# Optimization experiments

Hardware: AMD Instinct MI355X
Metric: run time of the kernel (lower is better)

The kernel has to match this reference:

```python
import jax, jax.numpy as jnp
from jax import lax
import numpy as np

B, C, H, W = 8, 192, 128, 128
HEADS, WS, SS = 6, 8, 4
HID = 768  # 4 * C
HEAD_DIM = C // HEADS
SCALE = HEAD_DIM ** -0.5
EPS = 1e-5


def _rel_pos_index(ws):
    coords = np.stack(np.meshgrid(np.arange(ws), np.arange(ws), indexing='ij'))  # (2, ws, ws)
    flat = coords.reshape(2, ws * ws)
    rel = flat[:, :, None] - flat[:, None, :]          # (2, N, N)
    rel = rel.transpose(1, 2, 0)                       # (N, N, 2)
    rel[:, :, 0] += ws - 1
    rel[:, :, 1] += ws - 1
    rel[:, :, 0] *= 2 * ws - 1
    return rel.sum(-1).astype(np.int32)                # (N, N)


def _attn_mask(hp, wp, ws, ss):
    # Swin shift mask: 0 where tokens share a region, -100 otherwise. (nW, N, N)
    img = np.zeros((hp, wp), dtype=np.float32)
    slices = (slice(0, -ws), slice(-ws, -ss), slice(-ss, None))
    cnt = 0
    for hs in slices:
        for ws_ in slices:
            img[hs, ws_] = float(cnt)
            cnt += 1
    mw = img.reshape(hp // ws, ws, wp // ws, ws).transpose(0, 2, 1, 3).reshape(-1, ws * ws)
    am = mw[:, None, :] - mw[:, :, None]
    return np.where(am != 0, -100.0, 0.0).astype(np.float32)


def _layernorm(x, g, b):
    mu = jnp.mean(x, axis=-1, keepdims=True)
    var = jnp.mean(jnp.square(x - mu), axis=-1, keepdims=True)
    return (x - mu) * lax.rsqrt(var + EPS) * g + b


def setup_inputs() -> dict:
    key = jax.random.key(0)
    ks = jax.random.split(key, 16)
    s = 0.02
    return {
        'x': jax.random.normal(ks[0], (B, C, H, W), jnp.float32),
        'pos_conv_w': jax.random.normal(ks[1], (C, 1, 3, 3), jnp.float32) * s,
        'norm1_g': jnp.ones((C,), jnp.float32),
        'norm1_b': jnp.zeros((C,), jnp.float32),
        'qkv_w': jax.random.normal(ks[2], (C, 3 * C), jnp.float32) * s,
        'qkv_b': jnp.zeros((3 * C,), jnp.float32),
        'proj_w': jax.random.normal(ks[3], (C, C), jnp.float32) * s,
        'proj_b': jnp.zeros((C,), jnp.float32),
        'rel_bias_table': jax.random.normal(ks[4], ((2 * WS - 1) ** 2, HEADS), jnp.float32) * s,
        'norm2_g': jnp.ones((C,), jnp.float32),
        'norm2_b': jnp.zeros((C,), jnp.float32),
        'mlp_w1': jax.random.normal(ks[5], (C, HID), jnp.float32) * s,
        'mlp_b1': jnp.zeros((HID,), jnp.float32),
        'mlp_w2': jax.random.normal(ks[6], (HID, C), jnp.float32) * s,
        'mlp_b2': jnp.zeros((C,), jnp.float32),
    }


def reference(x, pos_conv_w, norm1_g, norm1_b, qkv_w, qkv_b, proj_w, proj_b,
              rel_bias_table, norm2_g, norm2_b, mlp_w1, mlp_b1, mlp_w2, mlp_b2):
    b, c, h, w = x.shape
    ws, ss, nh, hd = WS, SS, HEADS, HEAD_DIM
    N = ws * ws

    # depthwise 3x3 positional conv (residual)
    x = x + lax.conv_general_dilated(
        x, pos_conv_w, (1, 1), 'SAME', feature_group_count=c,
        dimension_numbers=('NCHW', 'OIHW', 'NCHW'))

    if ss > 0:
        x = jnp.roll(x, (-ss, -ss), axis=(2, 3))

    pad_h = (ws - h % ws) % ws
    pad_w = (ws - w % ws) % ws
    if pad_h or pad_w:
        x = jnp.pad(x, ((0, 0), (0, 0), (0, pad_h), (0, pad_w)))
    hp, wp = h + pad_h, w + pad_w

    # window partition -> (num_windows, N, c)
    windows = x.reshape(b, c, hp // ws, ws, wp // ws, ws)
    windows = windows.transpose(0, 2, 4, 3, 5, 1).reshape(-1, N, c)
    nw = windows.shape[0]

    a = _layernorm(windows, norm1_g, norm1_b)
    qkv = (a @ qkv_w + qkv_b).reshape(nw, N, 3, nh, hd).transpose(2, 0, 3, 1, 4)
    q, k, v = qkv[0], qkv[1], qkv[2]                      # (nw, nh, N, hd)

    attn = jnp.einsum('whnd,whmd->whnm', q * SCALE, k)    # (nw, nh, N, N)

    rel_idx = jnp.asarray(_rel_pos_index(ws))             # (N, N) int
    bias = rel_bias_table[rel_idx.reshape(-1)].reshape(N, N, nh).transpose(2, 0, 1)
    attn = attn + bias[None]

    if ss > 0:
        mask = jnp.asarray(_attn_mask(hp, wp, ws, ss))    # (nW_per_img, N, N)
        nwpb = (hp // ws) * (wp // ws)
        attn = attn.reshape(b, nwpb, nh, N, N) + mask[None, :, None]
        attn = attn.reshape(nw, nh, N, N)

    attn = jax.nn.softmax(attn, axis=-1)
    out = jnp.einsum('whnm,whmd->whnd', attn, v).transpose(0, 2, 1, 3).reshape(nw, N, c)

    windows = windows + out @ proj_w + proj_b
    hmid = jax.nn.gelu(_layernorm(windows, norm2_g, norm2_b) @ mlp_w1 + mlp_b1, approximate=False)
    windows = windows + hmid @ mlp_w2 + mlp_b2

    # unpartition -> (b, c, hp, wp), crop, roll back
    y = windows.reshape(b, hp // ws, wp // ws, ws, ws, c)
    y = y.transpose(0, 5, 1, 3, 2, 4).reshape(b, c, hp, wp)[:, :, :h, :w]
    if ss > 0:
        y = jnp.roll(y, (ss, ss), axis=(2, 3))
    return y
```

## Files before the change

### kernel.cpp

```cpp
#include <hip/hip_runtime.h>
#include <hip/hip_bf16.h>
#include <cstdint>
#include <cstddef>

typedef short short8 __attribute__((ext_vector_type(8)));
typedef float float4_ __attribute__((ext_vector_type(4)));
typedef unsigned int uint4_ __attribute__((ext_vector_type(4)));
typedef unsigned int uint2_ __attribute__((ext_vector_type(2)));

#define DEVI static __device__ __forceinline__

DEVI unsigned short f2bf(float f) {
  union { float f; unsigned u; } v; v.f = f;
  return (unsigned short)((v.u + 0x7FFFu + ((v.u >> 16) & 1u)) >> 16);
}
DEVI unsigned pack2bf(float a, float b) {
  return (unsigned)f2bf(a) | ((unsigned)f2bf(b) << 16);
}
DEVI unsigned short f2bfc(float f) {
  __hip_bfloat16 h = __float2bfloat16(f);
  union { __hip_bfloat16 h1; unsigned short u; } cv; cv.h1 = h; return cv.u;
}
DEVI unsigned pack2bfc(float a, float b) {
  float2 f2; f2.x = a; f2.y = b;
  __hip_bfloat162 h = __float22bfloat162_rn(f2);
  union { __hip_bfloat162 h2; unsigned u; } cv; cv.h2 = h; return cv.u;
}
DEVI float bf2f(unsigned short h) {
  union { unsigned u; float f; } v; v.u = ((unsigned)h) << 16;
  return v.f;
}
DEVI float gelu_f(float x) {
  float u = x * (0.7978845608f + 0.0356774081f * x * x);
  float e = exp2f(-2.8853900818f * u);
  return x * __builtin_amdgcn_rcpf(1.0f + e);
}

#define SCALE_Q 0.17677669529663687f

__global__ __launch_bounds__(256) void k_prep(
    const float* __restrict__ qkv_w, const float* __restrict__ qkv_b,
    const float* __restrict__ proj_w, const float* __restrict__ mlp_w1,
    const float* __restrict__ mlp_w2, const float* __restrict__ relt,
    unsigned short* __restrict__ qkvWT, unsigned short* __restrict__ projWT,
    unsigned short* __restrict__ w1T, unsigned short* __restrict__ w2T,
    float* __restrict__ qkv_b_s, float* __restrict__ bias_attn) {
  int i = blockIdx.x * 256 + threadIdx.x;
  if (i < 110592) { int n = i / 192, k = i - n * 192;
    float v = qkv_w[k * 576 + n]; if (n < 192) v *= SCALE_Q;
    qkvWT[i] = f2bf(v); return; }
  i -= 110592;
  if (i < 576) { qkv_b_s[i] = qkv_b[i] * (i < 192 ? SCALE_Q : 1.0f); return; }
  i -= 576;
  if (i < 36864) { int n = i / 192, k = i - n * 192;
    projWT[i] = f2bf(proj_w[k * 192 + n]); return; }
  i -= 36864;
  if (i < 147456) { int n = i / 192, k = i - n * 192;
    w1T[i] = f2bf(mlp_w1[k * 768 + n]); return; }
  i -= 147456;
  if (i < 147456) { int n = i / 768, k = i - n * 768;
    w2T[i] = f2bf(mlp_w2[k * 192 + n]); return; }
  i -= 147456;
  if (i < 24576) {
    int h = i >> 12, nm = i & 4095, n = nm >> 6, m = nm & 63;
    int dr = (n >> 3) - (m >> 3) + 7, dc = (n & 7) - (m & 7) + 7;
    bias_attn[i] = relt[(dr * 15 + dc) * 6 + h];
  }
}

__global__ __launch_bounds__(256) void k_conv(
    const float* __restrict__ x, const float* __restrict__ convw,
    unsigned short* __restrict__ temp) {
  __shared__ float s_in[66 * 128];
  int bx = blockIdx.x;
  int c = bx >> 1, seg = bx & 1, b = blockIdx.y;
  int h0 = seg * 64;
  int t = threadIdx.x;
  const float* xp = x + ((size_t)(b * 192 + c)) * 16384;
  #pragma unroll
  for (int i = 0; i < 9; ++i) {
    int q = t + i * 256;
    if (q < 2112) {
      int srow = q >> 5, chunk = q & 31;
      float4_ v = *(const float4_*)(xp + ((h0 + 3 + srow) & 127) * 128 + chunk * 4);
      *(float4_*)(s_in + srow * 128 + chunk * 4) = v;
    }
  }
  float cw9[9];
  #pragma unroll
  for (int i = 0; i < 9; ++i) cw9[i] = convw[c * 9 + i];
  __syncthreads();
  int r2 = t >> 7;
  int wp = t & 127;
  int w_true = (wp + 4) & 127;
  float mw0 = (w_true != 0) ? 1.f : 0.f;
  float mw2 = (w_true != 127) ? 1.f : 0.f;
  int wl0 = (w_true + 127) & 127, wl2 = (w_true + 1) & 127;
  unsigned short* tp = temp + ((size_t)(b * 192 + c)) * 16384;
  #pragma unroll 4
  for (int it = 0; it < 32; ++it) {
    int r = it * 2 + r2;
    int h_true = (h0 + 4 + r) & 127;
    float mh0 = (h_true != 0) ? 1.f : 0.f;
    float mh2 = (h_true != 127) ? 1.f : 0.f;
    const float* row0 = s_in + r * 128;
    const float* row1 = row0 + 128;
    const float* row2 = row1 + 128;
    float acc = row1[w_true];
    acc = fmaf(cw9[0], mh0 * mw0 * row0[wl0], acc);
    acc = fmaf(cw9[1], mh0 * row0[w_true], acc);
    acc = fmaf(cw9[2], mh0 * mw2 * row0[wl2], acc);
    acc = fmaf(cw9[3], mw0 * row1[wl0], acc);
    acc = fmaf(cw9[4], row1[w_true], acc);
    acc = fmaf(cw9[5], mw2 * row1[wl2], acc);
    acc = fmaf(cw9[6], mh2 * mw0 * row2[wl0], acc);
    acc = fmaf(cw9[7], mh2 * row2[w_true], acc);
    acc = fmaf(cw9[8], mh2 * mw2 * row2[wl2], acc);
    tp[(size_t)(h0 + r) * 128 + wp] = f2bf(acc);
  }
}

__global__ __launch_bounds__(256) void k_lnw(
    const unsigned short* __restrict__ temp, const float* __restrict__ g1,
    const float* __restrict__ b1, unsigned short* __restrict__ xw,
    unsigned short* __restrict__ a) {
  __shared__ unsigned short sT[192 * 128];
  __shared__ float s_g[192], s_b[192];
  int t = threadIdx.x;
  for (int i = t; i < 192; i += 256) { s_g[i] = g1[i]; s_b[i] = b1[i]; }
  int wj0 = blockIdx.x * 2, wi = blockIdx.y, b = blockIdx.z;
  const unsigned short* tb = temp + (size_t)b * (192 * 16384) + (wi * 8) * 128 + wj0 * 8;
  #pragma unroll
  for (int i = 0; i < 12; ++i) {
    int id = t + i * 256;
    int c = id >> 4, rem = id & 15, r = rem >> 1, piece = rem & 1;
    short8 v = *(const short8*)(tb + (size_t)c * 16384 + r * 128 + piece * 8);
    *(short8*)(sT + c * 128 + piece * 64 + r * 8) = v;
  }
  __syncthreads();
  int tok = t >> 1, half = t & 1, c0 = half * 96;
  size_t gtok = ((size_t)(b * 256 + wi * 16 + wj0 + (tok >> 6))) * 64 + (tok & 63);
  unsigned short* xwp = xw + gtok * 192 + c0;
  float sum = 0.f, sq = 0.f;
  #pragma unroll
  for (int j8 = 0; j8 < 12; ++j8) {
    unsigned short raw[8];
    unsigned pk[4];
    #pragma unroll
    for (int e = 0; e < 8; ++e) {
      unsigned short rv = sT[(c0 + j8 * 8 + e) * 128 + tok];
      raw[e] = rv;
      float x = bf2f(rv);
      sum += x; sq = fmaf(x, x, sq);
    }
    #pragma unroll
    for (int k = 0; k < 4; ++k) pk[k] = (unsigned)raw[2 * k] | ((unsigned)raw[2 * k + 1] << 16);
    uint4_ pv = { pk[0], pk[1], pk[2], pk[3] };
    *(uint4_*)(xwp + j8 * 8) = pv;
  }
  sum += __shfl_xor(sum, 1);
  sq  += __shfl_xor(sq, 1);
  float mu = sum * (1.f / 192.f);
  float var = sq * (1.f / 192.f) - mu * mu;
  float rs = rsqrtf(var + 1e-5f);
  unsigned short* ap = a + gtok * 192 + c0;
  #pragma unroll
  for (int j8 = 0; j8 < 12; ++j8) {
    unsigned pk[4];
    #pragma unroll
    for (int k = 0; k < 4; ++k) {
      int c = c0 + j8 * 8 + k * 2;
      float v0 = (bf2f(sT[c * 128 + tok]) - mu) * rs * s_g[c] + s_b[c];
      float v1 = (bf2f(sT[(c + 1) * 128 + tok]) - mu) * rs * s_g[c + 1] + s_b[c + 1];
      pk[k] = pack2bf(v0, v1);
    }
    uint4_ pv = { pk[0], pk[1], pk[2], pk[3] };
    *(uint4_*)(ap + j8 * 8) = pv;
  }
}

__global__ __launch_bounds__(384, 1) void k_qkvattn(
    const unsigned short* __restrict__ a, const unsigned short* __restrict__ wT,
    const float* __restrict__ qbias, const float* __restrict__ biasAll,
    unsigned short* __restrict__ outO) {
  __shared__ __align__(16) unsigned short sQK[6][4096];
  __shared__ __align__(16) unsigned short sVT[6][2048];
  int t = threadIdx.x, lane = t & 63, head = t / 64;
  int win = blockIdx.x;
  int wi = (win >> 4) & 15, wj = win & 15;
  int lrow = lane & 15, lkgrp = lane >> 4, lk = lkgrp * 8;
  const unsigned short* aWin = a + (size_t)win * (64 * 192);
  char* qk = (char*)sQK[head];
  char* vt = (char*)sVT[head];

  auto gemmQKV = [&](int sel) {
    const unsigned short* wb = wT + (size_t)(sel * 192 + head * 32) * 192;
    const float* bb = qbias + sel * 192 + head * 32;
    short8 bw[2][6];
    #pragma unroll
    for (int nb = 0; nb < 2; ++nb)
      #pragma unroll
      for (int ks = 0; ks < 6; ++ks)
        bw[nb][ks] = *(const short8*)(wb + (size_t)(nb * 16 + lrow) * 192 + ks * 32 + lk);
    float4_ acc[2][4];
    #pragma unroll
    for (int nb = 0; nb < 2; ++nb)
      #pragma unroll
      for (int mi = 0; mi < 4; ++mi) acc[nb][mi] = (float4_){0.f, 0.f, 0.f, 0.f};
    short8 af0[4], af1[4];
    #pragma unroll
    for (int mi = 0; mi < 4; ++mi)
      af0[mi] = *(const short8*)(aWin + (size_t)(mi * 16 + lrow) * 192 + lk);
    #pragma unroll
    for (int mi = 0; mi < 4; ++mi)
      af1[mi] = *(const short8*)(aWin + (size_t)(mi * 16 + lrow) * 192 + 32 + lk);
    #pragma unroll
    for (int ks = 0; ks < 6; ++ks) {
      #pragma unroll
      for (int mi = 0; mi < 4; ++mi) {
        short8 a_ = (ks & 1) ? af1[mi] : af0[mi];
        #pragma unroll
        for (int nb = 0; nb < 2; ++nb)
          acc[nb][mi] = __builtin_amdgcn_mfma_f32_16x16x32_bf16(bw[nb][ks], a_, acc[nb][mi], 0, 0, 0);
      }
      if (ks < 4) {
        #pragma unroll
        for (int mi = 0; mi < 4; ++mi) {
          short8 nv = *(const short8*)(aWin + (size_t)(mi * 16 + lrow) * 192 + (ks + 2) * 32 + lk);
          if (ks & 1) af1[mi] = nv; else af0[mi] = nv;
        }
      }
    }
    #pragma unroll
    for (int nb = 0; nb < 2; ++nb) {
      float4_ b4 = *(const float4_*)(bb + nb * 16 + lkgrp * 4);
      if (sel == 2) {
        #pragma unroll
        for (int mi = 0; mi < 4; ++mi) {
          int tok = mi * 16 + lrow;
          #pragma unroll
          for (int e = 0; e < 4; ++e) {
            int d = nb * 16 + lkgrp * 4 + e;
            *(unsigned short*)(vt + ((d * 128 + tok * 2) ^ ((d & 7) << 4))) =
                f2bfc(acc[nb][mi][e] + b4[e]);
          }
        }
      } else {
        int dsub2 = (nb * 16 + lkgrp * 4) * 2;
        #pragma unroll
        for (int mi = 0; mi < 4; ++mi) {
          int tok = mi * 16 + lrow;
          uint2_ pv = { pack2bfc(acc[nb][mi][0] + b4[0], acc[nb][mi][1] + b4[1]),
                        pack2bfc(acc[nb][mi][2] + b4[2], acc[nb][mi][3] + b4[3]) };
          *(uint2_*)(qk + sel * 4096 + ((tok * 64 + dsub2) ^ ((tok & 7) << 4))) = pv;
        }
      }
    }
  };
  gemmQKV(0);
  gemmQKV(1);
  gemmQKV(2);

  short8 kf[4];
  #pragma unroll
  for (int ni = 0; ni < 4; ++ni) {
    int tokk = ni * 16 + lrow;
    kf[ni] = *(const short8*)(qk + 4096 + ((tokk * 64 + lk * 2) ^ ((tokk & 7) << 4)));
  }
  float4_ s[4][4];
  __builtin_amdgcn_s_setprio(1);
  #pragma unroll
  for (int mi = 0; mi < 4; ++mi) {
    int tokq = mi * 16 + lrow;
    short8 qf = *(const short8*)(qk + ((tokq * 64 + lk * 2) ^ ((tokq & 7) << 4)));
    #pragma unroll
    for (int ni = 0; ni < 4; ++ni) {
      s[mi][ni] = (float4_){0.f, 0.f, 0.f, 0.f};
      s[mi][ni] = __builtin_amdgcn_mfma_f32_16x16x32_bf16(qf, kf[ni], s[mi][ni], 0, 0, 0);
    }
  }
  __builtin_amdgcn_s_setprio(0);
  const float* bh = biasAll + head * 4096;
  bool wi15 = (wi == 15), wj15 = (wj == 15);
  bool edge = wi15 || wj15;
  #pragma unroll
  for (int mi = 0; mi < 4; ++mi) {
    #pragma unroll
    for (int e = 0; e < 4; ++e) {
      int row = mi * 16 + lkgrp * 4 + e;
      int rcls = (wi15 ? ((row >> 3) >= 4 ? 2 : 1) : 0) * 3 +
                 (wj15 ? ((row & 7) >= 4 ? 2 : 1) : 0);
      float v[4];
      #pragma unroll
      for (int ni = 0; ni < 4; ++ni) {
        int col = ni * 16 + lrow;
        float xv = s[mi][ni][e] + bh[row * 64 + col];
        if (edge) {
          int ccls = (wi15 ? ((col >> 3) >= 4 ? 2 : 1) : 0) * 3 +
                     (wj15 ? ((col & 7) >= 4 ? 2 : 1) : 0);
          if (ccls != rcls) xv -= 100.f;
        }
        v[ni] = xv;
      }
      float mx = fmaxf(fmaxf(v[0], v[1]), fmaxf(v[2], v[3]));
      mx = fmaxf(mx, __shfl_xor(mx, 1));
      mx = fmaxf(mx, __shfl_xor(mx, 2));
      mx = fmaxf(mx, __shfl_xor(mx, 4));
      mx = fmaxf(mx, __shfl_xor(mx, 8));
      float sm = 0.f;
      #pragma unroll
      for (int ni = 0; ni < 4; ++ni) { v[ni] = __expf(v[ni] - mx); sm += v[ni]; }
      sm += __shfl_xor(sm, 1);
      sm += __shfl_xor(sm, 2);
      sm += __shfl_xor(sm, 4);
      sm += __shfl_xor(sm, 8);
      float inv = 1.f / sm;
      #pragma unroll
      for (int ni = 0; ni < 4; ++ni) {
        int col = ni * 16 + lrow;
        *(unsigned short*)(qk + ((row * 128 + col * 2) ^ ((row & 7) << 4))) = f2bfc(v[ni] * inv);
      }
    }
  }
  float4_ o[2][4];
  #pragma unroll
  for (int db = 0; db < 2; ++db)
    #pragma unroll
    for (int qb2 = 0; qb2 < 4; ++qb2) o[db][qb2] = (float4_){0.f, 0.f, 0.f, 0.f};
  __builtin_amdgcn_s_setprio(1);
  #pragma unroll
  for (int kk = 0; kk < 2; ++kk) {
    int ktok = kk * 32 + lk;
    short8 vf[2], pf[4];
    #pragma unroll
    for (int db = 0; db < 2; ++db) {
      int d = db * 16 + lrow;
      vf[db] = *(const short8*)(vt + ((d * 128 + ktok * 2) ^ ((d & 7) << 4)));
    }
    #pragma unroll
    for (int qb2 = 0; qb2 < 4; ++qb2) {
      int rq = qb2 * 16 + lrow;
      pf[qb2] = *(const short8*)(qk + ((rq * 128 + ktok * 2) ^ ((rq & 7) << 4)));
    }
    #pragma unroll
    for (int db = 0; db < 2; ++db)
      #pragma unroll
      for (int qb2 = 0; qb2 < 4; ++qb2)
        o[db][qb2] = __builtin_amdgcn_mfma_f32_16x16x32_bf16(vf[db], pf[qb2], o[db][qb2], 0, 0, 0);
  }
  __builtin_amdgcn_s_setprio(0);
  unsigned short* ob = outO + (size_t)win * (64 * 192);
  #pragma unroll
  for (int qb2 = 0; qb2 < 4; ++qb2)
    #pragma unroll
    for (int db = 0; db < 2; ++db) {
      unsigned lo = pack2bfc(o[db][qb2][0], o[db][qb2][1]);
      unsigned hi = pack2bfc(o[db][qb2][2], o[db][qb2][3]);
      uint2_ pv = { lo, hi };
      *(uint2_*)(ob + (size_t)(qb2 * 16 + lrow) * 192 + head * 32 + db * 16 + lkgrp * 4) = pv;
    }
}

__global__ __launch_bounds__(256, 2) void k_mlp(
    const unsigned short* __restrict__ O, const unsigned short* __restrict__ xw,
    const unsigned short* __restrict__ projWT, const float* __restrict__ proj_b,
    const float* __restrict__ n2g, const float* __restrict__ n2b,
    const unsigned short* __restrict__ w1T, const float* __restrict__ mlpb1,
    const unsigned short* __restrict__ w2T, const float* __restrict__ mlpb2,
    float* __restrict__ y) {
  __shared__ __align__(16) unsigned short sH[64 * 192];
  __shared__ __align__(16) unsigned short sB2[64 * 192];
  __shared__ float sRed[64 * 8];
  __shared__ unsigned sTok[64];
  int t = threadIdx.x, lane = t & 63, wn = t >> 6;
  int lrow = lane & 15, lkgrp = lane >> 4, lk = lkgrp * 8;
  int blk = blockIdx.x;
  int b = blk >> 8, rem = blk & 255, ta = rem >> 3, tb_ = rem & 7;
  if (t < 64) {
    int rr = t >> 4, ss = t & 15;
    int h = ta * 4 + rr, w = tb_ * 16 + ss;
    int hp = (h + 124) & 127, wp = (w + 124) & 127;
    unsigned gtok = ((unsigned)(b * 256 + (hp >> 3) * 16 + (wp >> 3))) * 64 +
                    (hp & 7) * 8 + (wp & 7);
    sTok[t] = gtok * 192u;
  }
  __syncthreads();
  unsigned aoff[4];
  #pragma unroll
  for (int mi = 0; mi < 4; ++mi) aoff[mi] = sTok[mi * 16 + lrow];
  float4_ tacc[4][3];
  #pragma unroll
  for (int mi = 0; mi < 4; ++mi)
    #pragma unroll
    for (int ni = 0; ni < 3; ++ni) tacc[mi][ni] = (float4_){0.f, 0.f, 0.f, 0.f};
  {
    short8 bP0[3][3], bP1[3][3], af0[4], af1[4];
    #pragma unroll
    for (int ni = 0; ni < 3; ++ni)
      #pragma unroll
      for (int k3 = 0; k3 < 3; ++k3)
        bP0[ni][k3] = *(const short8*)(projWT + (size_t)(wn * 48 + ni * 16 + lrow) * 192 + k3 * 32 + lk);
    #pragma unroll
    for (int mi = 0; mi < 4; ++mi)
      af0[mi] = *(const short8*)(O + aoff[mi] + lk);
    #pragma unroll
    for (int ni = 0; ni < 3; ++ni)
      #pragma unroll
      for (int k3 = 0; k3 < 3; ++k3)
        bP1[ni][k3] = *(const short8*)(projWT + (size_t)(wn * 48 + ni * 16 + lrow) * 192 + (3 + k3) * 32 + lk);
    #pragma unroll
    for (int mi = 0; mi < 4; ++mi)
      af1[mi] = *(const short8*)(O + aoff[mi] + 32 + lk);
    #pragma unroll
    for (int ks = 0; ks < 6; ++ks) {
      #pragma unroll
      for (int mi = 0; mi < 4; ++mi) {
        short8 a_ = (ks & 1) ? af1[mi] : af0[mi];
        #pragma unroll
        for (int ni = 0; ni < 3; ++ni) {
          short8 b_ = (ks < 3) ? bP0[ni][ks] : bP1[ni][ks - 3];
          tacc[mi][ni] = __builtin_amdgcn_mfma_f32_16x16x32_bf16(a_, b_, tacc[mi][ni], 0, 0, 0);
        }
      }
      if (ks < 4) {
        #pragma unroll
        for (int mi = 0; mi < 4; ++mi) {
          short8 nv = *(const short8*)(O + aoff[mi] + (ks + 2) * 32 + lk);
          if (ks & 1) af1[mi] = nv; else af0[mi] = nv;
        }
      }
    }
  }
  {
    unsigned roff[4][4];
    #pragma unroll
    for (int mi = 0; mi < 4; ++mi)
      #pragma unroll
      for (int e = 0; e < 4; ++e)
        roff[mi][e] = sTok[mi * 16 + lkgrp * 4 + e];
    unsigned short rxv[3][4][4];
    #pragma unroll
    for (int ni = 0; ni < 3; ++ni) {
      int col = wn * 48 + ni * 16 + lrow;
      #pragma unroll
      for (int mi = 0; mi < 4; ++mi)
        #pragma unroll
        for (int e = 0; e < 4; ++e)
          rxv[ni][mi][e] = xw[roff[mi][e] + col];
    }
    #pragma unroll
    for (int ni = 0; ni < 3; ++ni) {
      float pbv = proj_b[wn * 48 + ni * 16 + lrow];
      #pragma unroll
      for (int mi = 0; mi < 4; ++mi)
        #pragma unroll
        for (int e = 0; e < 4; ++e)
          tacc[mi][ni][e] += pbv + bf2f(rxv[ni][mi][e]);
    }
  }
  #pragma unroll
  for (int mi = 0; mi < 4; ++mi)
    #pragma unroll
    for (int e = 0; e < 4; ++e) {
      float s1 = tacc[mi][0][e] + tacc[mi][1][e] + tacc[mi][2][e];
      float s2 = tacc[mi][0][e] * tacc[mi][0][e] + tacc[mi][1][e] * tacc[mi][1][e] +
                 tacc[mi][2][e] * tacc[mi][2][e];
      s1 += __shfl_xor(s1, 1); s1 += __shfl_xor(s1, 2); s1 += __shfl_xor(s1, 4); s1 += __shfl_xor(s1, 8);
      s2 += __shfl_xor(s2, 1); s2 += __shfl_xor(s2, 2); s2 += __shfl_xor(s2, 4); s2 += __shfl_xor(s2, 8);
      if (lrow == 0) {
        int row = mi * 16 + lkgrp * 4 + e;
        sRed[row * 8 + wn * 2 + 0] = s1;
        sRed[row * 8 + wn * 2 + 1] = s2;
      }
    }
  __syncthreads();
  #pragma unroll
  for (int mi = 0; mi < 4; ++mi)
    #pragma unroll
    for (int e = 0; e < 4; ++e) {
      int row = mi * 16 + lkgrp * 4 + e;
      float s1 = sRed[row * 8] + sRed[row * 8 + 2] + sRed[row * 8 + 4] + sRed[row * 8 + 6];
      float s2 = sRed[row * 8 + 1] + sRed[row * 8 + 3] + sRed[row * 8 + 5] + sRed[row * 8 + 7];
      float mu = s1 * (1.f / 192.f);
      float var = s2 * (1.f / 192.f) - mu * mu;
      float rs = rsqrtf(var + 1e-5f);
      #pragma unroll
      for (int ni = 0; ni < 3; ++ni) {
        int col = wn * 48 + ni * 16 + lrow;
        float hv = (tacc[mi][ni][e] - mu) * rs * n2g[col] + n2b[col];
        *(unsigned short*)((char*)sH + ((row * 384 + col * 2) ^ ((row & 7) << 4))) = f2bfc(hv);
      }
    }
  __syncthreads();
  short8 bwA[6], bwB[6];
  #pragma unroll
  for (int ks = 0; ks < 6; ++ks)
    bwA[ks] = *(const short8*)(w1T + (size_t)(wn * 48 + lrow) * 192 + ks * 32 + lk);
  #pragma unroll 1
  for (int ch = 0; ch < 4; ++ch) {
    #pragma unroll 1
    for (int ni = 0; ni < 3; ++ni) {
      int nni = (ni < 2) ? ni + 1 : 0;
      int nch = (ni < 2) ? ch : ch + 1;
      if (nch < 4) {
        int gn = nch * 192 + wn * 48 + nni * 16 + lrow;
        #pragma unroll
        for (int ks = 0; ks < 6; ++ks)
          bwB[ks] = *(const short8*)(w1T + (size_t)gn * 192 + ks * 32 + lk);
      }
      float4_ h1[4];
      #pragma unroll
      for (int mi = 0; mi < 4; ++mi) h1[mi] = (float4_){0.f, 0.f, 0.f, 0.f};
      __builtin_amdgcn_s_setprio(1);
      #pragma unroll
      for (int ks = 0; ks < 6; ++ks) {
        int kb = ks * 32 + lk;
        #pragma unroll
        for (int mi = 0; mi < 4; ++mi) {
          int row = mi * 16 + lrow;
          short8 afv = *(const short8*)((const char*)sH + ((row * 384 + kb * 2) ^ ((row & 7) << 4)));
          h1[mi] = __builtin_amdgcn_mfma_f32_16x16x32_bf16(bwA[ks], afv, h1[mi], 0, 0, 0);
        }
      }
      __builtin_amdgcn_s_setprio(0);
      float4_ b4 = *(const float4_*)(mlpb1 + ch * 192 + wn * 48 + ni * 16 + lkgrp * 4);
      int nsub2 = (wn * 48 + ni * 16 + lkgrp * 4) * 2;
      #pragma unroll
      for (int mi = 0; mi < 4; ++mi) {
        int tok_ = mi * 16 + lrow;
        float g0 = gelu_f(h1[mi][0] + b4[0]);
        float g1 = gelu_f(h1[mi][1] + b4[1]);
        float g2 = gelu_f(h1[mi][2] + b4[2]);
        float g3 = gelu_f(h1[mi][3] + b4[3]);
        uint2_ pv = { pack2bfc(g0, g1), pack2bfc(g2, g3) };
        *(uint2_*)((char*)sB2 + ((tok_ * 384 + nsub2) ^ ((tok_ & 7) << 4))) = pv;
      }
      #pragma unroll
      for (int ks = 0; ks < 6; ++ks) bwA[ks] = bwB[ks];
    }
    short8 cw0[3][3], cw1[3][3];
    #pragma unroll
    for (int ni = 0; ni < 3; ++ni)
      #pragma unroll
      for (int k3 = 0; k3 < 3; ++k3)
        cw0[ni][k3] = *(const short8*)(w2T + (size_t)(wn * 48 + ni * 16 + lrow) * 768 + ch * 192 + k3 * 32 + lk);
    __syncthreads();
    #pragma unroll
    for (int ni = 0; ni < 3; ++ni)
      #pragma unroll
      for (int k3 = 0; k3 < 3; ++k3)
        cw1[ni][k3] = *(const short8*)(w2T + (size_t)(wn * 48 + ni * 16 + lrow) * 768 + ch * 192 + (3 + k3) * 32 + lk);
    __builtin_amdgcn_s_setprio(1);
    #pragma unroll
    for (int ks = 0; ks < 6; ++ks) {
      int kb = ks * 32 + lk;
      short8 af[4];
      #pragma unroll
      for (int mi = 0; mi < 4; ++mi) {
        int row = mi * 16 + lrow;
        af[mi] = *(const short8*)((const char*)sB2 + ((row * 384 + kb * 2) ^ ((row & 7) << 4)));
      }
      #pragma unroll
      for (int mi = 0; mi < 4; ++mi)
        #pragma unroll
        for (int ni = 0; ni < 3; ++ni) {
          short8 b_ = (ks < 3) ? cw0[ni][ks] : cw1[ni][ks - 3];
          tacc[mi][ni] = __builtin_amdgcn_mfma_f32_16x16x32_bf16(af[mi], b_, tacc[mi][ni], 0, 0, 0);
        }
    }
    __builtin_amdgcn_s_setprio(0);
    __syncthreads();
  }
  int wcol = tb_ * 16 + lkgrp * 4;
  #pragma unroll
  for (int ni = 0; ni < 3; ++ni) {
    int col = wn * 48 + ni * 16 + lrow;
    float b2v = mlpb2[col];
    #pragma unroll
    for (int mi = 0; mi < 4; ++mi) {
      int h = ta * 4 + mi;
      float4_ vv;
      #pragma unroll
      for (int e = 0; e < 4; ++e) vv[e] = tacc[mi][ni][e] + b2v;
      *(float4_*)(y + ((size_t)(b * 192 + col) * 128 + h) * 128 + wcol) = vv;
    }
  }
}

extern "C" void kernel_launch(void* const* d_in, const int* in_sizes, int n_in,
                              void* d_out, int out_size, void* d_ws, size_t ws_size,
                              hipStream_t stream) {
  (void)in_sizes; (void)n_in; (void)out_size;
  const float* x    = (const float*)d_in[0];
  const float* pcw  = (const float*)d_in[1];
  const float* n1g  = (const float*)d_in[2];
  const float* n1b  = (const float*)d_in[3];
  const float* qkvw = (const float*)d_in[4];
  const float* qkvb = (const float*)d_in[5];
  const float* pw   = (const float*)d_in[6];
  const float* pb   = (const float*)d_in[7];
  const float* relt = (const float*)d_in[8];
  const float* n2g  = (const float*)d_in[9];
  const float* n2b  = (const float*)d_in[10];
  const float* w1   = (const float*)d_in[11];
  const float* mb1  = (const float*)d_in[12];
  const float* w2   = (const float*)d_in[13];
  const float* mb2  = (const float*)d_in[14];
  float* y = (float*)d_out;
  char* ws = (char*)d_ws;
  size_t off = 0;
  auto carve = [&](size_t bytes) { void* p = ws + off; off += (bytes + 255) & ~(size_t)255; return p; };
  unsigned short* qkvWT  = (unsigned short*)carve(576 * 192 * 2);
  unsigned short* projWT = (unsigned short*)carve(192 * 192 * 2);
  unsigned short* w1T    = (unsigned short*)carve(768 * 192 * 2);
  unsigned short* w2T    = (unsigned short*)carve(192 * 768 * 2);
  float* qkv_b_s   = (float*)carve(576 * 4);
  float* bias_attn = (float*)carve(6 * 64 * 64 * 4);
  unsigned short* aBuf   = (unsigned short*)carve((size_t)131072 * 192 * 2);
  unsigned short* xwBuf  = (unsigned short*)carve((size_t)131072 * 192 * 2);
  unsigned short* temp   = (unsigned short*)carve((size_t)131072 * 192 * 2);
  if (off > ws_size) return;

  k_prep<<<dim3(1827), dim3(256), 0, stream>>>(qkvw, qkvb, pw, w1, w2, relt,
                                               qkvWT, projWT, w1T, w2T, qkv_b_s, bias_attn);
  k_conv<<<dim3(384, 8), dim3(256), 0, stream>>>(x, pcw, temp);
  k_lnw<<<dim3(8, 16, 8), dim3(256), 0, stream>>>(temp, n1g, n1b, xwBuf, aBuf);
  k_qkvattn<<<dim3(2048), dim3(384), 0, stream>>>(aBuf, qkvWT, qkv_b_s, bias_attn, temp);
  k_mlp<<<dim3(2048), dim3(256), 0, stream>>>(temp, xwBuf, projWT, pb, n2g, n2b,
                                              w1T, mb1, w2T, mb2, y);
}
```

Measured before the change: 487.1 us.

## Split attention kernel into one-wave blocks per window-head, fuse Q/K/V GEMMs

The fused QKV+attention kernel now launches one 64-thread block per (window, head) instead of one 384-thread block per window with a wave per head. Each block keeps a single head's Q/K/V tile in shared memory, so less LDS is used per block and more blocks can be resident and scheduled independently. The three Q/K/V projections are merged into one K-loop that reuses each activation fragment across all six output tiles, cutting activation reloads. In exchange it holds 24 accumulators plus 12 weight fragments in registers, and the activation window is now loaded six times, once per head block.

```diff
diff --git a/kernel.cpp b/kernel.cpp
--- a/kernel.cpp
+++ b/kernel.cpp
@@ -179,87 +179,103 @@
   }
 }
 
-__global__ __launch_bounds__(384, 1) void k_qkvattn(
+__global__ __launch_bounds__(64, 2) void k_qkvattn(
     const unsigned short* __restrict__ a, const unsigned short* __restrict__ wT,
     const float* __restrict__ qbias, const float* __restrict__ biasAll,
     unsigned short* __restrict__ outO) {
-  __shared__ __align__(16) unsigned short sQK[6][4096];
-  __shared__ __align__(16) unsigned short sVT[6][2048];
-  int t = threadIdx.x, lane = t & 63, head = t / 64;
+  __shared__ __align__(16) unsigned short sQK[4096];
+  __shared__ __align__(16) unsigned short sVT[2048];
+  int lane = threadIdx.x;
+  int head = blockIdx.y;
   int win = blockIdx.x;
   int wi = (win >> 4) & 15, wj = win & 15;
   int lrow = lane & 15, lkgrp = lane >> 4, lk = lkgrp * 8;
   const unsigned short* aWin = a + (size_t)win * (64 * 192);
-  char* qk = (char*)sQK[head];
-  char* vt = (char*)sVT[head];
-
-  auto gemmQKV = [&](int sel) {
-    const unsigned short* wb = wT + (size_t)(sel * 192 + head * 32) * 192;
-    const float* bb = qbias + sel * 192 + head * 32;
-    short8 bw[2][6];
+  const unsigned short* wbase = wT + (size_t)head * 32 * 192;
+  char* qk = (char*)sQK;
+  char* vt = (char*)sVT;
+
+  float4_ acc[3][2][4];
+  #pragma unroll
+  for (int s = 0; s < 3; ++s)
     #pragma unroll
     for (int nb = 0; nb < 2; ++nb)
       #pragma unroll
-      for (int ks = 0; ks < 6; ++ks)
-        bw[nb][ks] = *(const short8*)(wb + (size_t)(nb * 16 + lrow) * 192 + ks * 32 + lk);
-    float4_ acc[2][4];
+      for (int mi = 0; mi < 4; ++mi) acc[s][nb][mi] = (float4_){0.f, 0.f, 0.f, 0.f};
+  short8 bwA[6], bwB[6], af0[4], af1[4];
+  #pragma unroll
+  for (int s = 0; s < 3; ++s)
     #pragma unroll
     for (int nb = 0; nb < 2; ++nb)
-      #pragma unroll
-      for (int mi = 0; mi < 4; ++mi) acc[nb][mi] = (float4_){0.f, 0.f, 0.f, 0.f};
-    short8 af0[4], af1[4];
-    #pragma unroll
-    for (int mi = 0; mi < 4; ++mi)
-      af0[mi] = *(const short8*)(aWin + (size_t)(mi * 16 + lrow) * 192 + lk);
-    #pragma unroll
-    for (int mi = 0; mi < 4; ++mi)
-      af1[mi] = *(const short8*)(aWin + (size_t)(mi * 16 + lrow) * 192 + 32 + lk);
-    #pragma unroll
-    for (int ks = 0; ks < 6; ++ks) {
+      bwA[s * 2 + nb] = *(const short8*)(wbase + (size_t)(s * 192 + nb * 16 + lrow) * 192 + lk);
+  #pragma unroll
+  for (int mi = 0; mi < 4; ++mi)
+    af0[mi] = *(const short8*)(aWin + (size_t)(mi * 16 + lrow) * 192 + lk);
+  #pragma unroll
+  for (int s = 0; s < 3; ++s)
+    #pragma unroll
+    for (int nb = 0; nb < 2; ++nb)
+      bwB[s * 2 + nb] = *(const short8*)(wbase + (size_t)(s * 192 + nb * 16 + lrow) * 192 + 32 + lk);
+  #pragma unroll
+  for (int mi = 0; mi < 4; ++mi)
+    af1[mi] = *(const short8*)(aWin + (size_t)(mi * 16 + lrow) * 192 + 32 + lk);
+  #pragma unroll
+  for (int ks = 0; ks < 6; ++ks) {
+    #pragma unroll
+    for (int mi = 0; mi < 4; ++mi) {
+      short8 a_ = (ks & 1) ? af1[mi] : af0[mi];
+      #pragma unroll
+      for (int sn = 0; sn < 6; ++sn) {
+        short8 b_ = (ks & 1) ? bwB[sn] : bwA[sn];
+        acc[sn >> 1][sn & 1][mi] =
+            __builtin_amdgcn_mfma_f32_16x16x32_bf16(b_, a_, acc[sn >> 1][sn & 1][mi], 0, 0, 0);
+      }
+    }
+    if (ks < 4) {
+      int kc = (ks + 2) * 32 + lk;
+      #pragma unroll
+      for (int s = 0; s < 3; ++s)
+        #pragma unroll
+        for (int nb = 0; nb < 2; ++nb) {
+          short8 nv = *(const short8*)(wbase + (size_t)(s * 192 + nb * 16 + lrow) * 192 + kc);
+          if (ks & 1) bwB[s * 2 + nb] = nv; else bwA[s * 2 + nb] = nv;
+        }
       #pragma unroll
       for (int mi = 0; mi < 4; ++mi) {
-        short8 a_ = (ks & 1) ? af1[mi] : af0[mi];
-        #pragma unroll
-        for (int nb = 0; nb < 2; ++nb)
-          acc[nb][mi] = __builtin_amdgcn_mfma_f32_16x16x32_bf16(bw[nb][ks], a_, acc[nb][mi], 0, 0, 0);
-      }
-      if (ks < 4) {
-        #pragma unroll
-        for (int mi = 0; mi < 4; ++mi) {
-          short8 nv = *(const short8*)(aWin + (size_t)(mi * 16 + lrow) * 192 + (ks + 2) * 32 + lk);
-          if (ks & 1) af1[mi] = nv; else af0[mi] = nv;
-        }
-      }
-    }
+        short8 nv = *(const short8*)(aWin + (size_t)(mi * 16 + lrow) * 192 + kc);
+        if (ks & 1) af1[mi] = nv; else af0[mi] = nv;
+      }
+    }
+  }
+  #pragma unroll
+  for (int sel = 0; sel < 2; ++sel) {
     #pragma unroll
     for (int nb = 0; nb < 2; ++nb) {
-      float4_ b4 = *(const float4_*)(bb + nb * 16 + lkgrp * 4);
-      if (sel == 2) {
-        #pragma unroll
-        for (int mi = 0; mi < 4; ++mi) {
-          int tok = mi * 16 + lrow;
-          #pragma unroll
-          for (int e = 0; e < 4; ++e) {
-            int d = nb * 16 + lkgrp * 4 + e;
-            *(unsigned short*)(vt + ((d * 128 + tok * 2) ^ ((d & 7) << 4))) =
-                f2bfc(acc[nb][mi][e] + b4[e]);
-          }
-        }
-      } else {
-        int dsub2 = (nb * 16 + lkgrp * 4) * 2;
-        #pragma unroll
-        for (int mi = 0; mi < 4; ++mi) {
-          int tok = mi * 16 + lrow;
-          uint2_ pv = { pack2bfc(acc[nb][mi][0] + b4[0], acc[nb][mi][1] + b4[1]),
-                        pack2bfc(acc[nb][mi][2] + b4[2], acc[nb][mi][3] + b4[3]) };
-          *(uint2_*)(qk + sel * 4096 + ((tok * 64 + dsub2) ^ ((tok & 7) << 4))) = pv;
-        }
-      }
-    }
-  };
-  gemmQKV(0);
-  gemmQKV(1);
-  gemmQKV(2);
+      float4_ b4 = *(const float4_*)(qbias + sel * 192 + head * 32 + nb * 16 + lkgrp * 4);
+      int dsub2 = (nb * 16 + lkgrp * 4) * 2;
+      #pragma unroll
+      for (int mi = 0; mi < 4; ++mi) {
+        int tok = mi * 16 + lrow;
+        uint2_ pv = { pack2bfc(acc[sel][nb][mi][0] + b4[0], acc[sel][nb][mi][1] + b4[1]),
+                      pack2bfc(acc[sel][nb][mi][2] + b4[2], acc[sel][nb][mi][3] + b4[3]) };
+        *(uint2_*)(qk + sel * 4096 + ((tok * 64 + dsub2) ^ ((tok & 7) << 4))) = pv;
+      }
+    }
+  }
+  #pragma unroll
+  for (int nb = 0; nb < 2; ++nb) {
+    float4_ b4 = *(const float4_*)(qbias + 384 + head * 32 + nb * 16 + lkgrp * 4);
+    #pragma unroll
+    for (int mi = 0; mi < 4; ++mi) {
+      int tok = mi * 16 + lrow;
+      #pragma unroll
+      for (int e = 0; e < 4; ++e) {
+        int d = nb * 16 + lkgrp * 4 + e;
+        *(unsigned short*)(vt + ((d * 128 + tok * 2) ^ ((d & 7) << 4))) =
+            f2bfc(acc[2][nb][mi][e] + b4[e]);
+      }
+    }
+  }
 
   short8 kf[4];
   #pragma unroll
@@ -625,7 +641,7 @@
                                                qkvWT, projWT, w1T, w2T, qkv_b_s, bias_attn);
   k_conv<<<dim3(384, 8), dim3(256), 0, stream>>>(x, pcw, temp);
   k_lnw<<<dim3(8, 16, 8), dim3(256), 0, stream>>>(temp, n1g, n1b, xwBuf, aBuf);
-  k_qkvattn<<<dim3(2048), dim3(384), 0, stream>>>(aBuf, qkvWT, qkv_b_s, bias_attn, temp);
+  k_qkvattn<<<dim3(2048, 6), dim3(64), 0, stream>>>(aBuf, qkvWT, qkv_b_s, bias_attn, temp);
   k_mlp<<<dim3(2048), dim3(256), 0, stream>>>(temp, xwBuf, projWT, pb, n2g, n2b,
                                               w1T, mb1, w2T, mb2, y);
 }
```

Result: no change. 496.7 us (+2.0%).
